# Optimization experiments

Hardware: AMD Instinct MI355X
Metric: run time of the kernel (lower is better)

Reference implementation:

```python
import jax, jax.numpy as jnp
import numpy as np
from jax import lax

V = 20000
NNZ = 640000
B, CIN, COUT, R = 16, 128, 128, 4


def setup_inputs() -> dict:
    key = jax.random.key(0)
    ks = jax.random.split(key, 6)
    x = jax.random.normal(ks[0], (B, CIN, V), dtype=jnp.float32)
    # kaiming-normal-like init, fan_in = R*CIN
    weight = jax.random.normal(ks[1], (R, CIN, COUT), dtype=jnp.float32) * np.float32(np.sqrt(2.0 / (R * CIN)))
    bias = jnp.full((COUT,), 0.01, dtype=jnp.float32)
    # sparse rescaled laplacian in COO format; values scaled small for stability
    lap_vals = jax.random.normal(ks[2], (NNZ,), dtype=jnp.float32) * np.float32(1.0 / 32.0)
    lap_rows = jax.random.randint(ks[3], (NNZ,), 0, V, dtype=jnp.int32)
    lap_cols = jax.random.randint(ks[4], (NNZ,), 0, V, dtype=jnp.int32)
    return {"x": x, "weight": weight, "bias": bias,
            "lap_vals": lap_vals, "lap_rows": lap_rows, "lap_cols": lap_cols}


def reference(x, weight, bias, lap_vals, lap_rows, lap_cols):
    # x: (B, Cin, V); weight: (R, Cin, Cout)
    Bd, Cin, Vd = x.shape
    Rd = weight.shape[0]

    def spmm(y):  # sparse (V,V) @ dense (V, F)
        return jax.ops.segment_sum(lap_vals[:, None] * y[lap_cols], lap_rows, num_segments=Vd)

    x0 = jnp.transpose(x, (2, 0, 1)).reshape(Vd, Bd * Cin)  # (V, B*Cin)
    if Rd > 1:
        x1 = spmm(x0)

        def step(carry, _):
            xm2, xm1 = carry
            xk = 2.0 * spmm(xm1) - xm2
            return (xm1, xk), xk

        if Rd > 2:
            _, rest = lax.scan(step, (x0, x1), None, length=Rd - 2)  # (R-2, V, B*Cin)
            xs = jnp.concatenate([x0[None], x1[None], rest], axis=0)
        else:
            xs = jnp.stack([x0, x1], axis=0)
    else:
        xs = x0[None]
    xs = xs.reshape(Rd, Vd, Bd, Cin)
    out = jnp.einsum('rvbi,rio->vbo', xs, weight) + bias  # (V, B, Cout)
    return jnp.transpose(out, (1, 2, 0))  # (B, Cout, V)
```

## Files before the change

kernel.cpp:

```cpp
#include <hip/hip_runtime.h>

#define V_N    20000
#define NNZ_N  640000
#define B_N    16
#define CIN_N  128
#define COUT_N 128
#define F_N    2048

typedef unsigned int u32;
typedef unsigned short u16;
typedef __attribute__((ext_vector_type(8))) short short8;
typedef __attribute__((ext_vector_type(4))) float floatx4;

__device__ __forceinline__ float bf_lo(u32 w) { return __uint_as_float(w << 16); }
__device__ __forceinline__ float bf_hi(u32 w) { return __uint_as_float(w & 0xffff0000u); }
__device__ __forceinline__ u16 f2bf(float f) {
    u32 u = __float_as_uint(f);
    u += 0x7fffu + ((u >> 16) & 1u);
    return (u16)(u >> 16);
}
__device__ __forceinline__ u32 pack2(float a, float b) {
    return (u32)f2bf(a) | ((u32)f2bf(b) << 16);
}

__device__ __forceinline__ void gload_lds16(const void* g, void* l)
{
    __builtin_amdgcn_global_load_lds(
        (const __attribute__((address_space(1))) u32*)g,
        (__attribute__((address_space(3))) u32*)l, 16, 0, 0);
}

__global__ __launch_bounds__(256) void k_transpose_f2h(const float* __restrict__ in,
                                                       u16* __restrict__ out,
                                                       int R, int C)
{
    __shared__ float tile[32][33];
    int cb = blockIdx.x * 32;
    int rb = blockIdx.y * 32;
    int tx = threadIdx.x, ty = threadIdx.y;
#pragma unroll
    for (int j = 0; j < 4; ++j) {
        int r = rb + ty + j * 8, c = cb + tx;
        if (r < R && c < C) tile[ty + j * 8][tx] = in[(size_t)r * C + c];
    }
    __syncthreads();
#pragma unroll
    for (int j = 0; j < 4; ++j) {
        int c = cb + ty + j * 8, r = rb + tx;
        if (r < R && c < C) out[(size_t)c * R + r] = f2bf(tile[tx][ty + j * 8]);
    }
}

__global__ __launch_bounds__(256) void k_hist(const int* __restrict__ rows,
                                              int* __restrict__ counts)
{
    int i = blockIdx.x * 256 + threadIdx.x;
    if (i < NNZ_N) atomicAdd(&counts[rows[i]], 1);
}

__global__ __launch_bounds__(1024) void k_scan(int* __restrict__ counts,
                                               int* __restrict__ row_ptr)
{
    const int C = 20;
    __shared__ int sd[1024];
    int t = threadIdx.x;
    int beg = t * C;
    int end = beg + C; if (end > V_N) end = V_N;
    if (beg > V_N) beg = V_N;
    int s = 0;
    for (int i = beg; i < end; ++i) s += counts[i];
    sd[t] = s;
    __syncthreads();
    for (int off = 1; off < 1024; off <<= 1) {
        int add = (t >= off) ? sd[t - off] : 0;
        __syncthreads();
        sd[t] += add;
        __syncthreads();
    }
    int run = sd[t] - s;
    for (int i = beg; i < end; ++i) {
        int cnt = counts[i];
        row_ptr[i] = run;
        counts[i]  = run;
        run += cnt;
    }
    if (t == 0) row_ptr[V_N] = NNZ_N;
}

__global__ __launch_bounds__(256) void k_scatter(const int* __restrict__ rows,
                                                 const int* __restrict__ cols_in,
                                                 const float* __restrict__ vals_in,
                                                 int* __restrict__ cursor,
                                                 int* __restrict__ csr_col,
                                                 float* __restrict__ csr_val)
{
    int i = blockIdx.x * 256 + threadIdx.x;
    if (i < NNZ_N) {
        int r = rows[i];
        int p = atomicAdd(&cursor[r], 1);
        csr_col[p] = cols_in[i];
        csr_val[p] = vals_in[i];
    }
}

__device__ __forceinline__ void acc8(float* acc, float s, uint4 q)
{
    acc[0] += s * bf_lo(q.x); acc[1] += s * bf_hi(q.x);
    acc[2] += s * bf_lo(q.y); acc[3] += s * bf_hi(q.y);
    acc[4] += s * bf_lo(q.z); acc[5] += s * bf_hi(q.z);
    acc[6] += s * bf_lo(q.w); acc[7] += s * bf_hi(q.w);
}

__global__ __launch_bounds__(256) void k_spmm_s(const u16* __restrict__ src,
                                                u16* __restrict__ dst,
                                                const u16* __restrict__ oldp,
                                                const int* __restrict__ row_ptr,
                                                const int* __restrict__ csr_col,
                                                const float* __restrict__ csr_val,
                                                int cheb)
{
    int n = blockIdx.x;
    int m = n >> 3;
    int slice = (n & 7) * 4 + m / 625;
    int chunk = m % 625;
    int tid = threadIdx.x;
    int sub = tid & 7;
    int v   = chunk * 32 + (tid >> 3);
    size_t fo = (size_t)slice * 64 + sub * 8;

    int jb = row_ptr[v], je = row_ptr[v + 1];
    float acc[8] = {0.f, 0.f, 0.f, 0.f, 0.f, 0.f, 0.f, 0.f};
    const u16* sp = src + fo;

    for (int j0 = jb; j0 < je; j0 += 8) {
        int idx = j0 + sub;
        int cc = 0; float vv = 0.f;
        if (idx < je) { cc = csr_col[idx]; vv = csr_val[idx]; }
        int nrem = je - j0;
        if (nrem >= 8) {
#pragma unroll
            for (int t = 0; t < 8; ++t) {
                int   col = __shfl(cc, t, 8);
                float s   = __shfl(vv, t, 8);
                uint4 q = *reinterpret_cast<const uint4*>(sp + (size_t)col * F_N);
                acc8(acc, s, q);
            }
        } else {
            for (int t = 0; t < nrem; ++t) {
                int   col = __shfl(cc, t, 8);
                float s   = __shfl(vv, t, 8);
                uint4 q = *reinterpret_cast<const uint4*>(sp + (size_t)col * F_N);
                acc8(acc, s, q);
            }
        }
    }

    u16* dp = dst + (size_t)v * F_N + fo;
    if (cheb) {
        uint4 oq = *reinterpret_cast<const uint4*>(oldp + (size_t)v * F_N + fo);
        float od[8];
        od[0] = bf_lo(oq.x); od[1] = bf_hi(oq.x);
        od[2] = bf_lo(oq.y); od[3] = bf_hi(oq.y);
        od[4] = bf_lo(oq.z); od[5] = bf_hi(oq.z);
        od[6] = bf_lo(oq.w); od[7] = bf_hi(oq.w);
#pragma unroll
        for (int t = 0; t < 8; ++t) acc[t] = 2.f * acc[t] - od[t];
    }
    uint4 o;
    o.x = pack2(acc[0], acc[1]);
    o.y = pack2(acc[2], acc[3]);
    o.z = pack2(acc[4], acc[5]);
    o.w = pack2(acc[6], acc[7]);
    *reinterpret_cast<uint4*>(dp) = o;
}

__global__ __launch_bounds__(256) void k_wprep(const float* __restrict__ w,
                                               u16* __restrict__ wt)
{
    int i = blockIdx.x * 256 + threadIdx.x;
    int o = i >> 9, k = i & 511;
    wt[i] = f2bf(w[(size_t)k * COUT_N + o]);
}

__global__ __launch_bounds__(256) void k_gemm_fused(const u16* __restrict__ h0,
                                                    const u16* __restrict__ h1,
                                                    const u16* __restrict__ h2,
                                                    const u16* __restrict__ h3,
                                                    const u16* __restrict__ wt,
                                                    const float* __restrict__ bias,
                                                    float* __restrict__ out)
{
    __shared__ __align__(16) u16 At[128 * 64];
    __shared__ __align__(16) u16 Wl[128 * 64];

    const u16* const planes[4] = {h0, h1, h2, h3};

    const int tid  = threadIdx.x;
    const int v0   = blockIdx.x * 128;
    const int b    = blockIdx.y;
    const int wave = tid >> 6;
    const int wm   = wave >> 1;
    const int wn   = wave & 1;
    const int l15  = tid & 15;
    const int l4   = (tid & 63) >> 4;

    const int srow = tid >> 3;
    const int sch  = tid & 7;

    floatx4 c[4][4];
#pragma unroll
    for (int fn = 0; fn < 4; ++fn) {
        float bo = bias[wn * 64 + fn * 16 + l15];
#pragma unroll
        for (int fm = 0; fm < 4; ++fm) c[fm][fn] = (floatx4){bo, bo, bo, bo};
    }

#pragma unroll
    for (int kt = 0; kt < 8; ++kt) {
        const u16* plane = planes[kt >> 1];
        const int  i0    = (kt & 1) * 64;
        const int  k0    = kt * 64;
        __syncthreads();
#pragma unroll
        for (int it = 0; it < 4; ++it) {
            int row = it * 32 + srow;
            int cch = sch ^ (row & 7);
            const u16* g = plane + (size_t)(v0 + row) * F_N + b * 128 + i0 + cch * 8;
            char* l = (char*)At + it * 4096 + (tid >> 6) * 1024;
            if (v0 + row < V_N) gload_lds16(g, l);
        }
#pragma unroll
        for (int it = 0; it < 4; ++it) {
            int row = it * 32 + srow;
            int cch = sch ^ (row & 7);
            const u16* g = wt + (size_t)row * 512 + k0 + cch * 8;
            char* l = (char*)Wl + it * 4096 + (tid >> 6) * 1024;
            gload_lds16(g, l);
        }
        __syncthreads();
#pragma unroll
        for (int k32 = 0; k32 < 2; ++k32) {
            short8 af[4], bf[4];
#pragma unroll
            for (int fm = 0; fm < 4; ++fm) {
                int row = wm * 64 + fm * 16 + l15;
                int ch  = k32 * 4 + l4;
                af[fm] = *reinterpret_cast<const short8*>(
                    (const char*)At + row * 128 + ((ch ^ (row & 7)) * 16));
            }
#pragma unroll
            for (int fn = 0; fn < 4; ++fn) {
                int row = wn * 64 + fn * 16 + l15;
                int ch  = k32 * 4 + l4;
                bf[fn] = *reinterpret_cast<const short8*>(
                    (const char*)Wl + row * 128 + ((ch ^ (row & 7)) * 16));
            }
#pragma unroll
            for (int fm = 0; fm < 4; ++fm)
#pragma unroll
                for (int fn = 0; fn < 4; ++fn)
                    c[fm][fn] = __builtin_amdgcn_mfma_f32_16x16x32_bf16(
                        af[fm], bf[fn], c[fm][fn], 0, 0, 0);
        }
    }

#pragma unroll
    for (int fm = 0; fm < 4; ++fm) {
        int v = v0 + wm * 64 + fm * 16 + l4 * 4;
        if (v < V_N) {
#pragma unroll
            for (int fn = 0; fn < 4; ++fn) {
                int o = wn * 64 + fn * 16 + l15;
                *reinterpret_cast<floatx4*>(out + (size_t)(b * 128 + o) * V_N + v) = c[fm][fn];
            }
        }
    }
}

extern "C" void kernel_launch(void* const* d_in, const int* in_sizes, int n_in,
                              void* d_out, int out_size, void* d_ws, size_t ws_size,
                              hipStream_t stream)
{
    const float* x        = (const float*)d_in[0];
    const float* weight   = (const float*)d_in[1];
    const float* bias     = (const float*)d_in[2];
    const float* lap_vals = (const float*)d_in[3];
    const int*   lap_rows = (const int*)d_in[4];
    const int*   lap_cols = (const int*)d_in[5];
    float* out = (float*)d_out;

    size_t plane = (size_t)V_N * F_N;
    u16* h0 = (u16*)d_ws;
    u16* h1 = h0 + plane;
    u16* h2 = h1 + plane;
    u16* h3 = h2 + plane;
    int*   counts  = (int*)(h3 + plane);
    int*   row_ptr = counts + V_N;
    int*   csr_col = row_ptr + V_N + 16;
    float* csr_val = (float*)(csr_col + NNZ_N);
    u16*   wt      = (u16*)csr_col;

    (void)hipMemsetAsync(counts, 0, V_N * sizeof(int), stream);
    k_hist<<<(NNZ_N + 255) / 256, 256, 0, stream>>>(lap_rows, counts);
    k_scan<<<1, 1024, 0, stream>>>(counts, row_ptr);
    k_scatter<<<(NNZ_N + 255) / 256, 256, 0, stream>>>(lap_rows, lap_cols, lap_vals,
                                                       counts, csr_col, csr_val);

    k_transpose_f2h<<<dim3(V_N / 32, F_N / 32), dim3(32, 8), 0, stream>>>(x, h0, F_N, V_N);

    k_spmm_s<<<V_N, 256, 0, stream>>>(h0, h1, (const u16*)0, row_ptr, csr_col, csr_val, 0);
    k_spmm_s<<<V_N, 256, 0, stream>>>(h1, h2, h0, row_ptr, csr_col, csr_val, 1);
    k_spmm_s<<<V_N, 256, 0, stream>>>(h2, h3, h1, row_ptr, csr_col, csr_val, 1);

    k_wprep<<<(512 * 128) / 256, 256, 0, stream>>>(weight, wt);
    k_gemm_fused<<<dim3((V_N + 127) / 128, B_N), 256, 0, stream>>>(
        h0, h1, h2, h3, wt, bias, out);
}
```

Before: 1.277 ms.

## Interleave CSR col/val pairs and have each lane load indices directly in SpMM

The scatter now writes column and value as one 8-byte pair, so the CSR data is a single interleaved array. In SpMM each lane loads the pairs itself instead of one cooperative load followed by shuffle broadcasts. The inner loop is unrolled by 4 with 32-bit byte offsets, packed float2 FMAs, and nontemporal loads and stores. A launch-bounds occupancy hint is added. Each lane now issues redundant pair loads, which should mostly hit the same cache lines, and the 32-bit offsets rely on the source plane offsets fitting in 32 bits.

```diff
diff --git a/kernel.cpp b/kernel.cpp
--- a/kernel.cpp
+++ b/kernel.cpp
@@ -11,6 +11,9 @@
 typedef unsigned short u16;
 typedef __attribute__((ext_vector_type(8))) short short8;
 typedef __attribute__((ext_vector_type(4))) float floatx4;
+typedef __attribute__((ext_vector_type(2))) float f32x2;
+typedef __attribute__((ext_vector_type(4))) u32 u32x4;
+typedef __attribute__((ext_vector_type(2))) int i32x2;
 
 __device__ __forceinline__ float bf_lo(u32 w) { return __uint_as_float(w << 16); }
 __device__ __forceinline__ float bf_hi(u32 w) { return __uint_as_float(w & 0xffff0000u); }
@@ -91,33 +94,34 @@
                                                  const int* __restrict__ cols_in,
                                                  const float* __restrict__ vals_in,
                                                  int* __restrict__ cursor,
-                                                 int* __restrict__ csr_col,
-                                                 float* __restrict__ csr_val)
+                                                 i32x2* __restrict__ pairs)
 {
     int i = blockIdx.x * 256 + threadIdx.x;
     if (i < NNZ_N) {
         int r = rows[i];
         int p = atomicAdd(&cursor[r], 1);
-        csr_col[p] = cols_in[i];
-        csr_val[p] = vals_in[i];
-    }
-}
-
-__device__ __forceinline__ void acc8(float* acc, float s, uint4 q)
-{
-    acc[0] += s * bf_lo(q.x); acc[1] += s * bf_hi(q.x);
-    acc[2] += s * bf_lo(q.y); acc[3] += s * bf_hi(q.y);
-    acc[4] += s * bf_lo(q.z); acc[5] += s * bf_hi(q.z);
-    acc[6] += s * bf_lo(q.w); acc[7] += s * bf_hi(q.w);
-}
-
-__global__ __launch_bounds__(256) void k_spmm_s(const u16* __restrict__ src,
-                                                u16* __restrict__ dst,
-                                                const u16* __restrict__ oldp,
-                                                const int* __restrict__ row_ptr,
-                                                const int* __restrict__ csr_col,
-                                                const float* __restrict__ csr_val,
-                                                int cheb)
+        i32x2 pr;
+        pr.x = cols_in[i];
+        pr.y = __float_as_int(vals_in[i]);
+        pairs[p] = pr;
+    }
+}
+
+__device__ __forceinline__ void acc4p(f32x2* a, f32x2 ss, u32x4 q)
+{
+    f32x2 w0 = {bf_lo(q.x), bf_hi(q.x)};
+    f32x2 w1 = {bf_lo(q.y), bf_hi(q.y)};
+    f32x2 w2 = {bf_lo(q.z), bf_hi(q.z)};
+    f32x2 w3 = {bf_lo(q.w), bf_hi(q.w)};
+    a[0] += ss * w0; a[1] += ss * w1; a[2] += ss * w2; a[3] += ss * w3;
+}
+
+__global__ __launch_bounds__(256, 6) void k_spmm_s(const u16* __restrict__ src,
+                                                   u16* __restrict__ dst,
+                                                   const u16* __restrict__ oldp,
+                                                   const int* __restrict__ row_ptr,
+                                                   const i32x2* __restrict__ pairs,
+                                                   int cheb)
 {
     int n = blockIdx.x;
     int m = n >> 3;
@@ -129,49 +133,59 @@
     size_t fo = (size_t)slice * 64 + sub * 8;
 
     int jb = row_ptr[v], je = row_ptr[v + 1];
-    float acc[8] = {0.f, 0.f, 0.f, 0.f, 0.f, 0.f, 0.f, 0.f};
-    const u16* sp = src + fo;
-
-    for (int j0 = jb; j0 < je; j0 += 8) {
-        int idx = j0 + sub;
-        int cc = 0; float vv = 0.f;
-        if (idx < je) { cc = csr_col[idx]; vv = csr_val[idx]; }
-        int nrem = je - j0;
-        if (nrem >= 8) {
-#pragma unroll
-            for (int t = 0; t < 8; ++t) {
-                int   col = __shfl(cc, t, 8);
-                float s   = __shfl(vv, t, 8);
-                uint4 q = *reinterpret_cast<const uint4*>(sp + (size_t)col * F_N);
-                acc8(acc, s, q);
-            }
-        } else {
-            for (int t = 0; t < nrem; ++t) {
-                int   col = __shfl(cc, t, 8);
-                float s   = __shfl(vv, t, 8);
-                uint4 q = *reinterpret_cast<const uint4*>(sp + (size_t)col * F_N);
-                acc8(acc, s, q);
-            }
-        }
+    f32x2 acc[4] = {{0.f, 0.f}, {0.f, 0.f}, {0.f, 0.f}, {0.f, 0.f}};
+
+    const char* base = (const char*)src + (size_t)slice * 128;
+    u32 subo = (u32)(sub * 16);
+
+    int j = jb;
+    for (; j + 4 <= je; j += 4) {
+        i32x2 p0 = __builtin_nontemporal_load(pairs + j);
+        i32x2 p1 = __builtin_nontemporal_load(pairs + j + 1);
+        i32x2 p2 = __builtin_nontemporal_load(pairs + j + 2);
+        i32x2 p3 = __builtin_nontemporal_load(pairs + j + 3);
+        u32 o0 = (((u32)p0.x) << 12) + subo;
+        u32 o1 = (((u32)p1.x) << 12) + subo;
+        u32 o2 = (((u32)p2.x) << 12) + subo;
+        u32 o3 = (((u32)p3.x) << 12) + subo;
+        u32x4 q0 = *reinterpret_cast<const u32x4*>(base + o0);
+        u32x4 q1 = *reinterpret_cast<const u32x4*>(base + o1);
+        u32x4 q2 = *reinterpret_cast<const u32x4*>(base + o2);
+        u32x4 q3 = *reinterpret_cast<const u32x4*>(base + o3);
+        f32x2 s0 = {__int_as_float(p0.y), __int_as_float(p0.y)};
+        f32x2 s1 = {__int_as_float(p1.y), __int_as_float(p1.y)};
+        f32x2 s2 = {__int_as_float(p2.y), __int_as_float(p2.y)};
+        f32x2 s3 = {__int_as_float(p3.y), __int_as_float(p3.y)};
+        acc4p(acc, s0, q0); acc4p(acc, s1, q1);
+        acc4p(acc, s2, q2); acc4p(acc, s3, q3);
+    }
+    for (; j < je; ++j) {
+        i32x2 p0 = __builtin_nontemporal_load(pairs + j);
+        u32 o0 = (((u32)p0.x) << 12) + subo;
+        u32x4 q0 = *reinterpret_cast<const u32x4*>(base + o0);
+        f32x2 s0 = {__int_as_float(p0.y), __int_as_float(p0.y)};
+        acc4p(acc, s0, q0);
     }
 
     u16* dp = dst + (size_t)v * F_N + fo;
     if (cheb) {
-        uint4 oq = *reinterpret_cast<const uint4*>(oldp + (size_t)v * F_N + fo);
-        float od[8];
-        od[0] = bf_lo(oq.x); od[1] = bf_hi(oq.x);
-        od[2] = bf_lo(oq.y); od[3] = bf_hi(oq.y);
-        od[4] = bf_lo(oq.z); od[5] = bf_hi(oq.z);
-        od[6] = bf_lo(oq.w); od[7] = bf_hi(oq.w);
-#pragma unroll
-        for (int t = 0; t < 8; ++t) acc[t] = 2.f * acc[t] - od[t];
-    }
-    uint4 o;
-    o.x = pack2(acc[0], acc[1]);
-    o.y = pack2(acc[2], acc[3]);
-    o.z = pack2(acc[4], acc[5]);
-    o.w = pack2(acc[6], acc[7]);
-    *reinterpret_cast<uint4*>(dp) = o;
+        u32x4 oq = __builtin_nontemporal_load(
+            reinterpret_cast<const u32x4*>(oldp + (size_t)v * F_N + fo));
+        f32x2 od0 = {bf_lo(oq.x), bf_hi(oq.x)};
+        f32x2 od1 = {bf_lo(oq.y), bf_hi(oq.y)};
+        f32x2 od2 = {bf_lo(oq.z), bf_hi(oq.z)};
+        f32x2 od3 = {bf_lo(oq.w), bf_hi(oq.w)};
+        acc[0] = 2.f * acc[0] - od0;
+        acc[1] = 2.f * acc[1] - od1;
+        acc[2] = 2.f * acc[2] - od2;
+        acc[3] = 2.f * acc[3] - od3;
+    }
+    u32x4 o;
+    o.x = pack2(acc[0].x, acc[0].y);
+    o.y = pack2(acc[1].x, acc[1].y);
+    o.z = pack2(acc[2].x, acc[2].y);
+    o.w = pack2(acc[3].x, acc[3].y);
+    __builtin_nontemporal_store(o, reinterpret_cast<u32x4*>(dp));
 }
 
 __global__ __launch_bounds__(256) void k_wprep(const float* __restrict__ w,
@@ -296,21 +310,20 @@
     u16* h3 = h2 + plane;
     int*   counts  = (int*)(h3 + plane);
     int*   row_ptr = counts + V_N;
-    int*   csr_col = row_ptr + V_N + 16;
-    float* csr_val = (float*)(csr_col + NNZ_N);
-    u16*   wt      = (u16*)csr_col;
+    i32x2* pairs   = (i32x2*)(row_ptr + V_N + 15);
+    u16*   wt      = (u16*)pairs;
 
     (void)hipMemsetAsync(counts, 0, V_N * sizeof(int), stream);
     k_hist<<<(NNZ_N + 255) / 256, 256, 0, stream>>>(lap_rows, counts);
     k_scan<<<1, 1024, 0, stream>>>(counts, row_ptr);
     k_scatter<<<(NNZ_N + 255) / 256, 256, 0, stream>>>(lap_rows, lap_cols, lap_vals,
-                                                       counts, csr_col, csr_val);
+                                                       counts, pairs);
 
     k_transpose_f2h<<<dim3(V_N / 32, F_N / 32), dim3(32, 8), 0, stream>>>(x, h0, F_N, V_N);
 
-    k_spmm_s<<<V_N, 256, 0, stream>>>(h0, h1, (const u16*)0, row_ptr, csr_col, csr_val, 0);
-    k_spmm_s<<<V_N, 256, 0, stream>>>(h1, h2, h0, row_ptr, csr_col, csr_val, 1);
-    k_spmm_s<<<V_N, 256, 0, stream>>>(h2, h3, h1, row_ptr, csr_col, csr_val, 1);
+    k_spmm_s<<<V_N, 256, 0, stream>>>(h0, h1, (const u16*)0, row_ptr, pairs, 0);
+    k_spmm_s<<<V_N, 256, 0, stream>>>(h1, h2, h0, row_ptr, pairs, 1);
+    k_spmm_s<<<V_N, 256, 0, stream>>>(h2, h3, h1, row_ptr, pairs, 1);
 
     k_wprep<<<(512 * 128) / 256, 256, 0, stream>>>(weight, wt);
     k_gemm_fused<<<dim3((V_N + 127) / 128, B_N), 256, 0, stream>>>(
```

After: 1.579 ms. 23.7% more time.
